# Optimization experiments

Measured on AMD Instinct MI355X. Metric: run time of the kernel, lower is better.

## Reference

```python
import jax, jax.numpy as jnp
import numpy as np

B, T, C, H = 2, 2048, 1024, 16
D = C // H  # head dim 64

def setup_inputs() -> dict:
    key = jax.random.key(0)
    k1, k2, k3 = jax.random.split(key, 3)
    x = jax.random.normal(k1, (B, T, C), dtype=jnp.float32)
    W_attn = jax.random.normal(k2, (C, 3 * C), dtype=jnp.float32) * (1.0 / np.sqrt(C))
    b_attn = jnp.zeros((3 * C,), dtype=jnp.float32)
    W_proj = jax.random.normal(k3, (C, C), dtype=jnp.float32) * (1.0 / np.sqrt(C))
    b_proj = jnp.zeros((C,), dtype=jnp.float32)
    return {"x": x, "W_attn": W_attn, "b_attn": b_attn, "W_proj": W_proj, "b_proj": b_proj}

def reference(x, W_attn, b_attn, W_proj, b_proj):
    Bsz, Tlen, Cdim = x.shape
    qkv = x @ W_attn + b_attn  # [B,T,3C]
    q, k, v = jnp.split(qkv, 3, axis=2)
    # [B,T,C] -> [B,H,T,D]
    q = q.reshape(Bsz, Tlen, H, D).transpose(0, 2, 1, 3)
    k = k.reshape(Bsz, Tlen, H, D).transpose(0, 2, 1, 3)
    v = v.reshape(Bsz, Tlen, H, D).transpose(0, 2, 1, 3)
    att = jnp.einsum('bhqd,bhkd->bhqk', q, k) * (1.0 / np.sqrt(D))
    causal = jnp.tril(jnp.ones((Tlen, Tlen), dtype=bool))
    att = jnp.where(causal[None, None, :, :], att, jnp.float32(-jnp.inf))
    att = jax.nn.softmax(att, axis=-1)
    y = jnp.einsum('bhqk,bhkd->bhqd', att, v)  # [B,H,T,D]
    y = y.transpose(0, 2, 1, 3).reshape(Bsz, Tlen, Cdim)
    return y @ W_proj + b_proj
```

## Files before the change

kernel.cpp:

```cpp
#include <hip/hip_runtime.h>
#include <math.h>

#define BSZ 2
#define TSEQ 2048
#define CDIM 1024
#define HNUM 16

typedef __attribute__((ext_vector_type(8))) short bhalf8;
typedef __attribute__((ext_vector_type(4))) short bhalf4;
typedef __attribute__((ext_vector_type(4))) float floatx4;

__device__ __forceinline__ unsigned short f2bf(float f) {
    union { float f; unsigned u; } v;
    v.f = f;
    unsigned r = v.u + 0x7FFFu + ((v.u >> 16) & 1u);
    return (unsigned short)(r >> 16);
}

typedef __attribute__((address_space(3))) unsigned int lds_u32;
typedef const __attribute__((address_space(1))) unsigned int g_u32;
__device__ __forceinline__ void async_copy16(const void* g, void* l) {
    __builtin_amdgcn_global_load_lds((g_u32*)g, (lds_u32*)l, 16, 0, 0);
}

__global__ __launch_bounds__(256) void conv_bf16(
    const float* __restrict__ x, unsigned short* __restrict__ xb)
{
    size_t i = ((size_t)blockIdx.x * 256 + threadIdx.x) * 8;
    float4 a = *(const float4*)(x + i);
    float4 b = *(const float4*)(x + i + 4);
    uint4 o;
    o.x = (unsigned)f2bf(a.x) | ((unsigned)f2bf(a.y) << 16);
    o.y = (unsigned)f2bf(a.z) | ((unsigned)f2bf(a.w) << 16);
    o.z = (unsigned)f2bf(b.x) | ((unsigned)f2bf(b.y) << 16);
    o.w = (unsigned)f2bf(b.z) | ((unsigned)f2bf(b.w) << 16);
    *(uint4*)(xb + i) = o;
}

__global__ __launch_bounds__(256) void transpose_bf16(
    const float* __restrict__ W, unsigned short* __restrict__ Wt, int K, int N)
{
    __shared__ float t[32][33];
    const int n0 = blockIdx.x * 32, k0 = blockIdx.y * 32;
    const int tx = threadIdx.x & 31, ty = threadIdx.x >> 5;
#pragma unroll
    for (int i = 0; i < 4; ++i)
        t[ty + i * 8][tx] = W[(size_t)(k0 + ty + i * 8) * N + n0 + tx];
    __syncthreads();
#pragma unroll
    for (int i = 0; i < 4; ++i)
        Wt[(size_t)(n0 + ty + i * 8) * K + k0 + tx] = f2bf(t[tx][ty + i * 8]);
}

template<bool OUT_BF16>
__global__ __launch_bounds__(256) void gemm_bt(
    const unsigned short* __restrict__ A, const unsigned short* __restrict__ Bt,
    const float* __restrict__ bias, void* __restrict__ Cp,
    int M, int N, int K, int v_start, unsigned short* __restrict__ vt)
{
    __shared__ unsigned short As[128 * 32];
    __shared__ unsigned short Bs[128 * 32];

    const int tid   = threadIdx.x;
    const int bm    = blockIdx.y;
    const int bn    = blockIdx.x;
    const int wave  = tid >> 6;
    const int col16 = tid & 15;
    const int quad  = (tid & 63) >> 4;
    const int wm    = (wave >> 1) * 64;
    const int wn    = (wave & 1) * 64;

    const floatx4 vzero = {0.f, 0.f, 0.f, 0.f};
    floatx4 acc[4][4];
#pragma unroll
    for (int i = 0; i < 4; ++i)
#pragma unroll
        for (int j = 0; j < 4; ++j) acc[i][j] = vzero;

    const int gr = tid >> 2;
    const int gk = (tid & 3) * 8;
    const unsigned short* Ab = A  + (size_t)(bm * 128 + gr) * K + gk;
    const unsigned short* Bb = Bt + (size_t)(bn * 128 + gr) * K + gk;
    char* AsB = (char*)As + wave * 1024;
    char* BsB = (char*)Bs + wave * 1024;

    for (int k0 = 0; k0 < K; k0 += 32) {
        __syncthreads();
        async_copy16(Ab + k0,          AsB);
        async_copy16(Ab + 64 * K + k0, AsB + 4096);
        async_copy16(Bb + k0,          BsB);
        async_copy16(Bb + 64 * K + k0, BsB + 4096);
        __syncthreads();

        bhalf8 a[4], b[4];
#pragma unroll
        for (int i = 0; i < 4; ++i)
            a[i] = *(const bhalf8*)&As[(wm + i * 16 + col16) * 32 + quad * 8];
#pragma unroll
        for (int j = 0; j < 4; ++j)
            b[j] = *(const bhalf8*)&Bs[(wn + j * 16 + col16) * 32 + quad * 8];
#pragma unroll
        for (int i = 0; i < 4; ++i)
#pragma unroll
            for (int j = 0; j < 4; ++j)
                acc[i][j] = __builtin_amdgcn_mfma_f32_16x16x32_bf16(a[i], b[j], acc[i][j], 0, 0, 0);
    }

    const int colbase = bn * 128 + wn;
    const bool vpath = (v_start >= 0) && (colbase >= v_start);
#pragma unroll
    for (int j = 0; j < 4; ++j) {
        int col = colbase + j * 16 + col16;
        float bv = bias[col];
#pragma unroll
        for (int i = 0; i < 4; ++i) {
#pragma unroll
            for (int r = 0; r < 4; ++r) {
                int row = bm * 128 + wm + i * 16 + quad * 4 + r;
                float v = acc[i][j][r] + bv;
                if (vpath) {
                    size_t vrow = (size_t)((row >> 11) * 1024 + (col - v_start));
                    vt[vrow * 2048 + (row & 2047)] = f2bf(v);
                } else if (OUT_BF16) {
                    ((unsigned short*)Cp)[(size_t)row * N + col] = f2bf(v);
                } else {
                    ((float*)Cp)[(size_t)row * N + col] = v;
                }
            }
        }
    }
}

__device__ __forceinline__ floatx4 fx4_zero() { floatx4 z = {0.f,0.f,0.f,0.f}; return z; }

template<bool DIAG>
__device__ __forceinline__ void attn_kv_tile(
    int kb,
    const unsigned short* __restrict__ kbase,
    const unsigned short* __restrict__ vtb,
    unsigned short* Ks, unsigned short* Vt,
    const bhalf8* qf, floatx4* oT, float& l_part,
    int tid, int col16, int quad, int qloc)
{
    const float C_MUL = 0.125f * 1.44269504f;
    const float C_SUB = 17.31234049f;

    const int krow0 = tid >> 3;
    const int kcb   = (tid & 7) ^ ((tid >> 3) & 7);
    char* ksb = (char*)Ks + (tid >> 6) * 1024;
    const int vc8s  = (tid & 7) ^ ((tid >> 3) & 7);
    char* vsb = (char*)Vt + (tid >> 6) * 1024;

    __syncthreads();
    async_copy16(kbase + (size_t)(kb * 64 + krow0) * 3072 + kcb * 8, ksb);
    async_copy16(kbase + (size_t)(kb * 64 + 32 + krow0) * 3072 + kcb * 8, ksb + 4096);
    async_copy16(vtb + (size_t)krow0 * 2048 + kb * 64 + vc8s * 8, vsb);
    async_copy16(vtb + (size_t)(krow0 + 32) * 2048 + kb * 64 + vc8s * 8, vsb + 4096);
    __syncthreads();

    const int sx = col16 & 7;
    floatx4 s[4];
#pragma unroll
    for (int n = 0; n < 4; ++n) {
        const int row = 16 * n + col16;
        bhalf8 k0 = *(const bhalf8*)&Ks[row * 64 + ((quad ^ sx) * 8)];
        bhalf8 k1 = *(const bhalf8*)&Ks[row * 64 + (((4 + quad) ^ sx) * 8)];
        floatx4 t = __builtin_amdgcn_mfma_f32_16x16x32_bf16(k0, qf[0], fx4_zero(), 0, 0, 0);
        s[n] = __builtin_amdgcn_mfma_f32_16x16x32_bf16(k1, qf[1], t, 0, 0, 0);
    }

    bhalf4 pb[4];
#pragma unroll
    for (int n = 0; n < 4; ++n) {
        unsigned a[4];
#pragma unroll
        for (int r = 0; r < 4; ++r) {
            float p = exp2f(fmaf(s[n][r], C_MUL, -C_SUB));
            if (DIAG) {
                const int kvloc = 16 * n + quad * 4 + r;
                if (kvloc > qloc) p = 0.f;
            }
            l_part += p;
            a[r] = __float_as_uint(p) + 0x8000u;
        }
        union { unsigned u[2]; bhalf4 b; } uu;
        uu.u[0] = (a[0] >> 16) | (a[1] & 0xffff0000u);
        uu.u[1] = (a[2] >> 16) | (a[3] & 0xffff0000u);
        pb[n] = uu.b;
    }

#pragma unroll
    for (int n = 0; n < 4; ++n) {
        const int ch = 2 * n + (quad >> 1);
#pragma unroll
        for (int dt = 0; dt < 4; ++dt) {
            const int d = 16 * dt + col16;
            bhalf4 av = *(const bhalf4*)&Vt[d * 64 + ((ch ^ (d & 7)) * 8) + (quad & 1) * 4];
            oT[dt] = __builtin_amdgcn_mfma_f32_16x16x16bf16_1k(av, pb[n], oT[dt], 0, 0, 0);
        }
    }
}

__global__ __launch_bounds__(256) void attn_mfma(
    const unsigned short* __restrict__ qkv,
    const unsigned short* __restrict__ vT,
    unsigned short* __restrict__ yout)
{
    __shared__ unsigned short Ks[64 * 64];
    __shared__ unsigned short Vt[64 * 64];

    const int tid   = threadIdx.x;
    const int wave  = tid >> 6;
    const int col16 = tid & 15;
    const int quad  = (tid & 63) >> 4;
    const int qb    = (int)gridDim.y - 1 - (int)blockIdx.y;
    const int bh    = blockIdx.x;
    const int b     = bh >> 4;
    const int h     = bh & 15;

    const unsigned short* base  = qkv + (size_t)b * TSEQ * 3072 + h * 64;
    const unsigned short* kbase = base + CDIM;
    const unsigned short* vtb   = vT + (size_t)(b * 1024 + h * 64) * 2048;

    bhalf8 qf[2];
    {
        const unsigned short* qrow =
            base + (size_t)(qb * 64 + wave * 16 + col16) * 3072 + quad * 8;
        qf[0] = *(const bhalf8*)qrow;
        qf[1] = *(const bhalf8*)(qrow + 32);
    }

    floatx4 oT[4];
#pragma unroll
    for (int dt = 0; dt < 4; ++dt) oT[dt] = fx4_zero();
    float l_part = 0.f;
    const int qloc = wave * 16 + col16;

    for (int kb = 0; kb < qb; ++kb)
        attn_kv_tile<false>(kb, kbase, vtb, Ks, Vt, qf, oT, l_part,
                            tid, col16, quad, qloc);
    attn_kv_tile<true>(qb, kbase, vtb, Ks, Vt, qf, oT, l_part,
                       tid, col16, quad, qloc);

    float l = l_part;
    l += __shfl_xor(l, 16);
    l += __shfl_xor(l, 32);
    const float inv = 1.0f / l;
    const size_t row = (size_t)b * TSEQ + (size_t)qb * 64 + wave * 16 + col16;
#pragma unroll
    for (int dt = 0; dt < 4; ++dt) {
        ushort4 o;
        o.x = f2bf(oT[dt][0] * inv);
        o.y = f2bf(oT[dt][1] * inv);
        o.z = f2bf(oT[dt][2] * inv);
        o.w = f2bf(oT[dt][3] * inv);
        *(ushort4*)(yout + row * CDIM + h * 64 + 16 * dt + quad * 4) = o;
    }
}

extern "C" void kernel_launch(void* const* d_in, const int* in_sizes, int n_in,
                              void* d_out, int out_size, void* d_ws, size_t ws_size,
                              hipStream_t stream)
{
    const float* x      = (const float*)d_in[0];
    const float* W_attn = (const float*)d_in[1];
    const float* b_attn = (const float*)d_in[2];
    const float* W_proj = (const float*)d_in[3];
    const float* b_proj = (const float*)d_in[4];
    float* out = (float*)d_out;

    unsigned short* qkv = (unsigned short*)d_ws;
    unsigned short* y   = qkv + (size_t)4096 * 3072;
    unsigned short* xb  = y   + (size_t)4096 * 1024;
    unsigned short* WtA = xb  + (size_t)4096 * 1024;
    unsigned short* WtP = WtA + (size_t)3072 * 1024;
    unsigned short* vT  = WtP + (size_t)1024 * 1024;

    conv_bf16<<<dim3((4096 * 1024) / (256 * 8)), 256, 0, stream>>>(x, xb);
    transpose_bf16<<<dim3(3072 / 32, 1024 / 32), 256, 0, stream>>>(W_attn, WtA, 1024, 3072);
    transpose_bf16<<<dim3(1024 / 32, 1024 / 32), 256, 0, stream>>>(W_proj, WtP, 1024, 1024);

    gemm_bt<true><<<dim3(3072 / 128, 4096 / 128), 256, 0, stream>>>(
        xb, WtA, b_attn, qkv, 4096, 3072, 1024, 2048, vT);
    attn_mfma<<<dim3(BSZ * HNUM, TSEQ / 64), 256, 0, stream>>>(qkv, vT, y);
    gemm_bt<false><<<dim3(1024 / 128, 4096 / 128), 256, 0, stream>>>(
        y, WtP, b_proj, out, 4096, 1024, 1024, -1, nullptr);
}
```

Measured before the change: 205.7 us.

## Double-buffer GEMM and attention loads, add separate V transpose, shrink proj tile

Both the GEMM and the attention kernels now use two LDS buffers, so the async global-to-LDS copy of the next K/V or A/B tile is issued before computing on the current one, with one barrier per iteration instead of two. The strided scattered V-transpose store in the QKV GEMM epilogue is replaced by a separate LDS-tiled vtrans kernel that writes coalesced rows. The V LDS layout changes to a rotated scheme to avoid bank conflicts. The output projection uses 64-row tiles to launch more blocks. The cost is an extra kernel launch plus an extra pass over V, and doubled LDS per block, which may lower occupancy.

```diff
diff --git a/kernel.cpp b/kernel.cpp
--- a/kernel.cpp
+++ b/kernel.cpp
@@ -16,6 +16,8 @@
     unsigned r = v.u + 0x7FFFu + ((v.u >> 16) & 1u);
     return (unsigned short)(r >> 16);
 }
+
+__device__ __forceinline__ floatx4 fx4_zero() { floatx4 z = {0.f,0.f,0.f,0.f}; return z; }
 
 typedef __attribute__((address_space(3))) unsigned int lds_u32;
 typedef const __attribute__((address_space(1))) unsigned int g_u32;
@@ -52,14 +54,52 @@
         Wt[(size_t)(n0 + ty + i * 8) * K + k0 + tx] = f2bf(t[tx][ty + i * 8]);
 }
 
-template<bool OUT_BF16>
+__global__ __launch_bounds__(256) void vtrans(
+    const unsigned short* __restrict__ qkv, unsigned short* __restrict__ vT)
+{
+    __shared__ unsigned short tt[64][80];
+    const int b  = blockIdx.z;
+    const int ty = blockIdx.y * 64;
+    const int cx = blockIdx.x * 64;
+    const int tid = threadIdx.x;
+    const int lr = tid >> 2, lc = (tid & 3) * 16;
+
+    const unsigned short* src =
+        qkv + (size_t)(b * 2048 + ty + lr) * 3072 + 2048 + cx + lc;
+    uint4 v0 = *(const uint4*)src;
+    uint4 v1 = *(const uint4*)(src + 8);
+    tt[lc + 0][lr]  = (unsigned short)(v0.x & 0xffff);
+    tt[lc + 1][lr]  = (unsigned short)(v0.x >> 16);
+    tt[lc + 2][lr]  = (unsigned short)(v0.y & 0xffff);
+    tt[lc + 3][lr]  = (unsigned short)(v0.y >> 16);
+    tt[lc + 4][lr]  = (unsigned short)(v0.z & 0xffff);
+    tt[lc + 5][lr]  = (unsigned short)(v0.z >> 16);
+    tt[lc + 6][lr]  = (unsigned short)(v0.w & 0xffff);
+    tt[lc + 7][lr]  = (unsigned short)(v0.w >> 16);
+    tt[lc + 8][lr]  = (unsigned short)(v1.x & 0xffff);
+    tt[lc + 9][lr]  = (unsigned short)(v1.x >> 16);
+    tt[lc + 10][lr] = (unsigned short)(v1.y & 0xffff);
+    tt[lc + 11][lr] = (unsigned short)(v1.y >> 16);
+    tt[lc + 12][lr] = (unsigned short)(v1.z & 0xffff);
+    tt[lc + 13][lr] = (unsigned short)(v1.z >> 16);
+    tt[lc + 14][lr] = (unsigned short)(v1.w & 0xffff);
+    tt[lc + 15][lr] = (unsigned short)(v1.w >> 16);
+    __syncthreads();
+    unsigned short* dst = vT + (size_t)(b * 1024 + cx + lr) * 2048 + ty + lc;
+    *(uint4*)dst       = *(const uint4*)&tt[lr][lc];
+    *(uint4*)(dst + 8) = *(const uint4*)&tt[lr][lc + 8];
+}
+
+template<int BM, bool OUT_BF16>
 __global__ __launch_bounds__(256) void gemm_bt(
     const unsigned short* __restrict__ A, const unsigned short* __restrict__ Bt,
     const float* __restrict__ bias, void* __restrict__ Cp,
-    int M, int N, int K, int v_start, unsigned short* __restrict__ vt)
-{
-    __shared__ unsigned short As[128 * 32];
-    __shared__ unsigned short Bs[128 * 32];
+    int M, int N, int K)
+{
+    constexpr int ALINES = BM / 64;
+    constexpr int MT = BM / 32;
+    __shared__ unsigned short As[2][BM * 32];
+    __shared__ unsigned short Bs[2][128 * 32];
 
     const int tid   = threadIdx.x;
     const int bm    = blockIdx.y;
@@ -67,98 +107,85 @@
     const int wave  = tid >> 6;
     const int col16 = tid & 15;
     const int quad  = (tid & 63) >> 4;
-    const int wm    = (wave >> 1) * 64;
+    const int wm    = (wave >> 1) * (BM / 2);
     const int wn    = (wave & 1) * 64;
 
-    const floatx4 vzero = {0.f, 0.f, 0.f, 0.f};
-    floatx4 acc[4][4];
-#pragma unroll
-    for (int i = 0; i < 4; ++i)
-#pragma unroll
-        for (int j = 0; j < 4; ++j) acc[i][j] = vzero;
+    floatx4 acc[MT][4];
+#pragma unroll
+    for (int i = 0; i < MT; ++i)
+#pragma unroll
+        for (int j = 0; j < 4; ++j) acc[i][j] = fx4_zero();
 
     const int gr = tid >> 2;
     const int gk = (tid & 3) * 8;
-    const unsigned short* Ab = A  + (size_t)(bm * 128 + gr) * K + gk;
+    const unsigned short* Ab = A  + (size_t)(bm * BM + gr) * K + gk;
     const unsigned short* Bb = Bt + (size_t)(bn * 128 + gr) * K + gk;
-    char* AsB = (char*)As + wave * 1024;
-    char* BsB = (char*)Bs + wave * 1024;
-
-    for (int k0 = 0; k0 < K; k0 += 32) {
+
+#define STAGE(k0, bf) { \
+    char* AsB = (char*)As[bf] + wave * 1024; \
+    char* BsB = (char*)Bs[bf] + wave * 1024; \
+    _Pragma("unroll") \
+    for (int l = 0; l < ALINES; ++l) \
+        async_copy16(Ab + (size_t)l * 64 * K + (k0), AsB + l * 4096); \
+    async_copy16(Bb + (k0), BsB); \
+    async_copy16(Bb + (size_t)64 * K + (k0), BsB + 4096); }
+
+#define COMPUTE(bf) { \
+    bhalf8 a[MT], b[4]; \
+    _Pragma("unroll") \
+    for (int i = 0; i < MT; ++i) \
+        a[i] = *(const bhalf8*)&As[bf][(wm + i * 16 + col16) * 32 + quad * 8]; \
+    _Pragma("unroll") \
+    for (int j = 0; j < 4; ++j) \
+        b[j] = *(const bhalf8*)&Bs[bf][(wn + j * 16 + col16) * 32 + quad * 8]; \
+    _Pragma("unroll") \
+    for (int i = 0; i < MT; ++i) \
+        _Pragma("unroll") \
+        for (int j = 0; j < 4; ++j) \
+            acc[i][j] = __builtin_amdgcn_mfma_f32_16x16x32_bf16(a[i], b[j], acc[i][j], 0, 0, 0); }
+
+    STAGE(0, 0);
+    __syncthreads();
+    int buf = 0;
+    for (int k0 = 0; k0 < K - 32; k0 += 32) {
+        STAGE(k0 + 32, buf ^ 1);
+        COMPUTE(buf);
         __syncthreads();
-        async_copy16(Ab + k0,          AsB);
-        async_copy16(Ab + 64 * K + k0, AsB + 4096);
-        async_copy16(Bb + k0,          BsB);
-        async_copy16(Bb + 64 * K + k0, BsB + 4096);
-        __syncthreads();
-
-        bhalf8 a[4], b[4];
-#pragma unroll
-        for (int i = 0; i < 4; ++i)
-            a[i] = *(const bhalf8*)&As[(wm + i * 16 + col16) * 32 + quad * 8];
-#pragma unroll
-        for (int j = 0; j < 4; ++j)
-            b[j] = *(const bhalf8*)&Bs[(wn + j * 16 + col16) * 32 + quad * 8];
-#pragma unroll
-        for (int i = 0; i < 4; ++i)
-#pragma unroll
-            for (int j = 0; j < 4; ++j)
-                acc[i][j] = __builtin_amdgcn_mfma_f32_16x16x32_bf16(a[i], b[j], acc[i][j], 0, 0, 0);
-    }
-
-    const int colbase = bn * 128 + wn;
-    const bool vpath = (v_start >= 0) && (colbase >= v_start);
+        buf ^= 1;
+    }
+    COMPUTE(buf);
+#undef STAGE
+#undef COMPUTE
+
 #pragma unroll
     for (int j = 0; j < 4; ++j) {
-        int col = colbase + j * 16 + col16;
+        int col = bn * 128 + wn + j * 16 + col16;
         float bv = bias[col];
 #pragma unroll
-        for (int i = 0; i < 4; ++i) {
+        for (int i = 0; i < MT; ++i) {
 #pragma unroll
             for (int r = 0; r < 4; ++r) {
-                int row = bm * 128 + wm + i * 16 + quad * 4 + r;
+                int row = bm * BM + wm + i * 16 + quad * 4 + r;
                 float v = acc[i][j][r] + bv;
-                if (vpath) {
-                    size_t vrow = (size_t)((row >> 11) * 1024 + (col - v_start));
-                    vt[vrow * 2048 + (row & 2047)] = f2bf(v);
-                } else if (OUT_BF16) {
+                if (OUT_BF16)
                     ((unsigned short*)Cp)[(size_t)row * N + col] = f2bf(v);
-                } else {
+                else
                     ((float*)Cp)[(size_t)row * N + col] = v;
-                }
             }
         }
     }
 }
 
-__device__ __forceinline__ floatx4 fx4_zero() { floatx4 z = {0.f,0.f,0.f,0.f}; return z; }
-
 template<bool DIAG>
-__device__ __forceinline__ void attn_kv_tile(
-    int kb,
-    const unsigned short* __restrict__ kbase,
-    const unsigned short* __restrict__ vtb,
-    unsigned short* Ks, unsigned short* Vt,
+__device__ __forceinline__ void attn_tile(
+    const unsigned short* __restrict__ Ks, const unsigned short* __restrict__ Vt,
     const bhalf8* qf, floatx4* oT, float& l_part,
-    int tid, int col16, int quad, int qloc)
+    int col16, int quad, int qloc)
 {
     const float C_MUL = 0.125f * 1.44269504f;
     const float C_SUB = 17.31234049f;
-
-    const int krow0 = tid >> 3;
-    const int kcb   = (tid & 7) ^ ((tid >> 3) & 7);
-    char* ksb = (char*)Ks + (tid >> 6) * 1024;
-    const int vc8s  = (tid & 7) ^ ((tid >> 3) & 7);
-    char* vsb = (char*)Vt + (tid >> 6) * 1024;
-
-    __syncthreads();
-    async_copy16(kbase + (size_t)(kb * 64 + krow0) * 3072 + kcb * 8, ksb);
-    async_copy16(kbase + (size_t)(kb * 64 + 32 + krow0) * 3072 + kcb * 8, ksb + 4096);
-    async_copy16(vtb + (size_t)krow0 * 2048 + kb * 64 + vc8s * 8, vsb);
-    async_copy16(vtb + (size_t)(krow0 + 32) * 2048 + kb * 64 + vc8s * 8, vsb + 4096);
-    __syncthreads();
-
     const int sx = col16 & 7;
+
     floatx4 s[4];
 #pragma unroll
     for (int n = 0; n < 4; ++n) {
@@ -177,8 +204,7 @@
         for (int r = 0; r < 4; ++r) {
             float p = exp2f(fmaf(s[n][r], C_MUL, -C_SUB));
             if (DIAG) {
-                const int kvloc = 16 * n + quad * 4 + r;
-                if (kvloc > qloc) p = 0.f;
+                if (16 * n + quad * 4 + r > qloc) p = 0.f;
             }
             l_part += p;
             a[r] = __float_as_uint(p) + 0x8000u;
@@ -191,11 +217,11 @@
 
 #pragma unroll
     for (int n = 0; n < 4; ++n) {
-        const int ch = 2 * n + (quad >> 1);
 #pragma unroll
         for (int dt = 0; dt < 4; ++dt) {
             const int d = 16 * dt + col16;
-            bhalf4 av = *(const bhalf4*)&Vt[d * 64 + ((ch ^ (d & 7)) * 8) + (quad & 1) * 4];
+            const bhalf4 av = *(const bhalf4*)
+                &Vt[n * 1024 + ((d + n) & 63) * 16 + (quad >> 1) * 8 + (quad & 1) * 4];
             oT[dt] = __builtin_amdgcn_mfma_f32_16x16x16bf16_1k(av, pb[n], oT[dt], 0, 0, 0);
         }
     }
@@ -206,8 +232,8 @@
     const unsigned short* __restrict__ vT,
     unsigned short* __restrict__ yout)
 {
-    __shared__ unsigned short Ks[64 * 64];
-    __shared__ unsigned short Vt[64 * 64];
+    __shared__ unsigned short Kbuf[2][64 * 64];
+    __shared__ unsigned short Vbuf[2][64 * 64];
 
     const int tid   = threadIdx.x;
     const int wave  = tid >> 6;
@@ -230,17 +256,44 @@
         qf[1] = *(const bhalf8*)(qrow + 32);
     }
 
+    const int krow = tid >> 3;
+    const int kchk = (tid & 7) ^ (krow & 7);
+    const unsigned short* ksrc0 = kbase + (size_t)krow * 3072 + kchk * 8;
+    const unsigned short* ksrc1 = kbase + (size_t)(krow + 32) * 3072 + kchk * 8;
+
+    int L0 = tid, L1 = tid + 256;
+    const int d0 = (((L0 >> 1) & 63) - ((L0 >> 1) >> 6)) & 63;
+    const int c0 = 2 * ((L0 >> 1) >> 6) + (L0 & 1);
+    const int d1 = (((L1 >> 1) & 63) - ((L1 >> 1) >> 6)) & 63;
+    const int c1 = 2 * ((L1 >> 1) >> 6) + (L1 & 1);
+    const unsigned short* vsrc0 = vtb + (size_t)d0 * 2048 + c0 * 8;
+    const unsigned short* vsrc1 = vtb + (size_t)d1 * 2048 + c1 * 8;
+
+#define ASTAGE(kb, bf) { \
+    char* Kd = (char*)Kbuf[bf] + wave * 1024; \
+    char* Vd = (char*)Vbuf[bf] + wave * 1024; \
+    async_copy16(ksrc0 + (size_t)(kb) * 64 * 3072, Kd); \
+    async_copy16(ksrc1 + (size_t)(kb) * 64 * 3072, Kd + 4096); \
+    async_copy16(vsrc0 + (kb) * 64, Vd); \
+    async_copy16(vsrc1 + (kb) * 64, Vd + 4096); }
+
     floatx4 oT[4];
 #pragma unroll
     for (int dt = 0; dt < 4; ++dt) oT[dt] = fx4_zero();
     float l_part = 0.f;
     const int qloc = wave * 16 + col16;
 
-    for (int kb = 0; kb < qb; ++kb)
-        attn_kv_tile<false>(kb, kbase, vtb, Ks, Vt, qf, oT, l_part,
-                            tid, col16, quad, qloc);
-    attn_kv_tile<true>(qb, kbase, vtb, Ks, Vt, qf, oT, l_part,
-                       tid, col16, quad, qloc);
+    ASTAGE(0, 0);
+    __syncthreads();
+    int buf = 0;
+    for (int kb = 0; kb < qb; ++kb) {
+        ASTAGE(kb + 1, buf ^ 1);
+        attn_tile<false>(Kbuf[buf], Vbuf[buf], qf, oT, l_part, col16, quad, qloc);
+        __syncthreads();
+        buf ^= 1;
+    }
+    attn_tile<true>(Kbuf[buf], Vbuf[buf], qf, oT, l_part, col16, quad, qloc);
+#undef ASTAGE
 
     float l = l_part;
     l += __shfl_xor(l, 16);
@@ -280,9 +333,10 @@
     transpose_bf16<<<dim3(3072 / 32, 1024 / 32), 256, 0, stream>>>(W_attn, WtA, 1024, 3072);
     transpose_bf16<<<dim3(1024 / 32, 1024 / 32), 256, 0, stream>>>(W_proj, WtP, 1024, 1024);
 
-    gemm_bt<true><<<dim3(3072 / 128, 4096 / 128), 256, 0, stream>>>(
-        xb, WtA, b_attn, qkv, 4096, 3072, 1024, 2048, vT);
+    gemm_bt<128, true><<<dim3(3072 / 128, 4096 / 128), 256, 0, stream>>>(
+        xb, WtA, b_attn, qkv, 4096, 3072, 1024);
+    vtrans<<<dim3(16, 32, 2), 256, 0, stream>>>(qkv, vT);
     attn_mfma<<<dim3(BSZ * HNUM, TSEQ / 64), 256, 0, stream>>>(qkv, vT, y);
-    gemm_bt<false><<<dim3(1024 / 128, 4096 / 128), 256, 0, stream>>>(
-        y, WtP, b_proj, out, 4096, 1024, 1024, -1, nullptr);
-}
+    gemm_bt<64, false><<<dim3(1024 / 128, 4096 / 64), 256, 0, stream>>>(
+        y, WtP, b_proj, out, 4096, 1024, 1024);
+}
```

Result: faster. 198.1 us (-3.7%).
